# Optimization experiments

Hardware: AMD Instinct MI355X
Metric: run time of the kernel (lower is better)

The kernel has to match this reference:

```python
import jax, jax.numpy as jnp
import numpy as np
from jax import lax

H = 160; W = 160
D_MODEL = 128; D_INNER = 512; D_STATE = 256; NHEADS = 16; HEADDIM = 32
D_CONV = 4; CHUNK = 64
CONV_DIM = D_INNER + 2 * D_STATE            # 1024
D_IN_PROJ = 2 * D_INNER + 2 * D_STATE + NHEADS  # 1552
EPS = 1e-5


def setup_inputs() -> dict:
    key = jax.random.key(0)
    ks = jax.random.split(key, 8)
    nrm = lambda k, s, sc: jax.random.normal(k, s, jnp.float32) * sc
    return {
        "x": jax.random.normal(ks[0], (1, 3, H, W), jnp.float32),
        "fc0_w": nrm(ks[1], (D_MODEL, 3), 0.3),
        "fc0_b": jnp.zeros((D_MODEL,), jnp.float32),
        "in_proj_w": nrm(ks[2], (D_IN_PROJ, D_MODEL), D_MODEL ** -0.5),
        "conv_w": nrm(ks[3], (CONV_DIM, D_CONV), 0.3),
        "conv_b": jnp.zeros((CONV_DIM,), jnp.float32),
        "dt_bias": jnp.log(jnp.expm1(jax.random.uniform(ks[4], (NHEADS,), minval=0.001, maxval=0.1))),
        "A_log": jnp.log(jax.random.uniform(ks[5], (NHEADS,), minval=1.0, maxval=16.0)),
        "D": jnp.ones((NHEADS,), jnp.float32),
        "norm_w": jnp.ones((D_INNER,), jnp.float32),
        "out_proj_w": nrm(ks[6], (D_MODEL, D_INNER), D_INNER ** -0.5),
        "fc1_w": nrm(ks[7], (D_MODEL, H * W), (H * W) ** -0.5),
        "fc1_b": jnp.zeros((D_MODEL,), jnp.float32),
    }


def segsum(x):
    # x: (..., T) -> (..., T, T) with out[i,j] = sum_{j < d <= i} x[d], -inf above diag
    T = x.shape[-1]
    strict = jnp.tril(jnp.ones((T, T), dtype=bool), -1)
    xx = jnp.where(strict, x[..., :, None], 0.0)
    cs = jnp.cumsum(xx, axis=-2)
    keep = jnp.tril(jnp.ones((T, T), dtype=bool))
    return jnp.where(keep, cs, -jnp.inf)


def ssd(xh, A, Bm, Cm):
    # xh: (b,l,h,p) already multiplied by dt; A: (b,l,h) = dt*A_head; Bm,Cm: (b,l,n) (ngroups=1)
    b, l, h, p = xh.shape
    n = Bm.shape[-1]
    c, q = l // CHUNK, CHUNK
    xh = xh.reshape(b, c, q, h, p)
    A = A.reshape(b, c, q, h).transpose(0, 3, 1, 2)          # (b,h,c,q)
    Bm = Bm.reshape(b, c, q, n)
    Cm = Cm.reshape(b, c, q, n)
    A_cs = jnp.cumsum(A, axis=-1)                            # (b,h,c,q)
    Lmat = jnp.exp(segsum(A))                                # (b,h,c,q,q)
    # intra-chunk (quadratic attention-like) term
    Y_diag = jnp.einsum('bcln,bcsn,bhcls,bcshp->bclhp', Cm, Bm, Lmat, xh)
    # per-chunk final states
    decay = jnp.exp(A_cs[..., -1:] - A_cs)                   # (b,h,c,q)
    states = jnp.einsum('bcln,bhcl,bclhp->bchpn', Bm, decay, xh)
    # inter-chunk recurrence: state entering each chunk
    a_tot = jnp.exp(A_cs[..., -1])                           # (b,h,c)
    def step(carry, inp):
        a_c, s_c = inp                                       # (b,h), (b,h,p,n)
        return a_c[..., None, None] * carry + s_c, carry
    _, states_in = lax.scan(step, jnp.zeros((b, h, p, n), xh.dtype),
                            (jnp.moveaxis(a_tot, 2, 0), jnp.moveaxis(states, 1, 0)))
    states_in = jnp.moveaxis(states_in, 0, 1)                # (b,c,h,p,n)
    Y_off = jnp.einsum('bcln,bchpn,bhcl->bclhp', Cm, states_in, jnp.exp(A_cs))
    return (Y_diag + Y_off).reshape(b, l, h, p)


def _forward(x, fc0_w, fc0_b, in_proj_w, conv_w, conv_b, dt_bias, A_log, D,
             norm_w, out_proj_w, fc1_w, fc1_b):
    b = x.shape[0]
    hw = H * W
    # bidirectional pixel flattening
    x1 = x.transpose(0, 2, 3, 1).reshape(b, hw, 3)
    x2 = x[:, :, ::-1, ::-1].transpose(0, 2, 3, 1).reshape(b, hw, 3)
    xc = jnp.concatenate([x1, x2], axis=1)                   # (b, 2*hw, 3)
    u = xc @ fc0_w.T + fc0_b                                 # (b, L, 128)
    L = u.shape[1]
    # Mamba2 in_proj
    zxbcdt = u @ in_proj_w.T                                 # (b, L, 1552)
    z = zxbcdt[..., :D_INNER]
    xBC = zxbcdt[..., D_INNER:D_INNER + CONV_DIM]
    dt = jax.nn.softplus(zxbcdt[..., D_INNER + CONV_DIM:] + dt_bias)  # (b, L, 16)
    # causal depthwise conv1d + silu
    conv = lax.conv_general_dilated(xBC.transpose(0, 2, 1), conv_w[:, None, :],
                                    (1,), [(D_CONV - 1, 0)],
                                    feature_group_count=CONV_DIM,
                                    dimension_numbers=('NCH', 'OIH', 'NCH'))
    xBC = jax.nn.silu(conv + conv_b[None, :, None]).transpose(0, 2, 1)
    xh = xBC[..., :D_INNER].reshape(b, L, NHEADS, HEADDIM)
    Bm = xBC[..., D_INNER:D_INNER + D_STATE]
    Cm = xBC[..., D_INNER + D_STATE:]
    A = -jnp.exp(A_log)                                      # (16,)
    Y = ssd(xh * dt[..., None], dt * A, Bm, Cm)
    Y = Y + D[None, None, :, None] * xh                      # skip connection
    y = Y.reshape(b, L, D_INNER)
    # gated RMSNorm (norm_before_gate=False)
    y = y * jax.nn.silu(z)
    y = y * lax.rsqrt(jnp.mean(y * y, axis=-1, keepdims=True) + EPS) * norm_w
    out = y @ out_proj_w.T                                   # (b, L, 128)
    # second half of sequence, mean over feature dim (AdaptiveAvgPool1d(1))
    half = out[:, hw:, :].mean(axis=-1)                      # (b, hw)
    return half @ fc1_w.T + fc1_b                            # (b, 128)


def reference(x, fc0_w, fc0_b, in_proj_w, conv_w, conv_b, dt_bias, A_log, D,
              norm_w, out_proj_w, fc1_w, fc1_b):
    return _forward(x, fc0_w, fc0_b, in_proj_w, conv_w, conv_b, dt_bias, A_log,
                    D, norm_w, out_proj_w, fc1_w, fc1_b)
```

## Files before the change

kernel.cpp:

```cpp
#include <hip/hip_runtime.h>

#define H_ 160
#define W_ 160
#define HW 25600
#define L_ 51200
#define DM 128
#define DI 512
#define DS 256
#define NH 16
#define HD 32
#define CONVD 1024
#define DIP 1552
#define NCH 800
#define NCH2 400
#define EPSV 1e-5f

typedef __attribute__((ext_vector_type(8))) short bf16x8;
typedef __attribute__((ext_vector_type(8))) unsigned short us8;
typedef __attribute__((ext_vector_type(4))) unsigned short us4;
typedef __attribute__((ext_vector_type(4))) float f32x4;
#define MFMA16(a,b,c) __builtin_amdgcn_mfma_f32_16x16x32_bf16(a,b,c,0,0,0)

__device__ __forceinline__ float b2f(unsigned short u){
  union{unsigned int i; float f;} v; v.i = ((unsigned int)u) << 16; return v.f;
}
__device__ __forceinline__ unsigned short f2b(float f){
  union{unsigned int i; float f;} v; v.f = f;
  unsigned int r = v.i + 0x7fffu + ((v.i >> 16) & 1u);
  return (unsigned short)(r >> 16);
}

__global__ void k_coef(const float* __restrict__ opw, const float* __restrict__ nw,
                       float* __restrict__ coef){
  int i = blockIdx.x * blockDim.x + threadIdx.x;
  if (i >= DI) return;
  float s = 0.f;
  for (int j = 0; j < DM; ++j) s += opw[j * DI + i];
  coef[i] = (s / (float)DM) * nw[i];
}

__global__ __launch_bounds__(256) void k_qtab(const float* __restrict__ ipw,
    const float* __restrict__ fw, const float* __restrict__ fb, float* __restrict__ q){
  int j = blockIdx.x * 256 + threadIdx.x;
  if (j >= DIP) return;
  const float* wr = ipw + (size_t)j * DM;
  float s0 = 0.f, s1 = 0.f, s2 = 0.f, sb = 0.f;
  for (int k = 0; k < DM; ++k){
    float w = wr[k];
    s0 += w * fw[k*3+0]; s1 += w * fw[k*3+1]; s2 += w * fw[k*3+2]; sb += w * fb[k];
  }
  reinterpret_cast<float4*>(q)[j] = make_float4(s0, s1, s2, sb);
}

__device__ __forceinline__ void xrow(const float* __restrict__ x, int l, float* o){
  int i, j;
  if (l < HW){ i = l / W_; j = l % W_; }
  else { int l2 = l - HW; i = (H_ - 1) - l2 / W_; j = (W_ - 1) - l2 % W_; }
  int p = i * W_ + j;
  o[0] = x[p]; o[1] = x[HW + p]; o[2] = x[2*HW + p];
}

__global__ __launch_bounds__(256) void k_fused(const float* __restrict__ x,
    const float* __restrict__ q, const float* __restrict__ cw, const float* __restrict__ cb,
    const float* __restrict__ dt_bias,
    unsigned short* __restrict__ g, unsigned short* __restrict__ xbc, float* __restrict__ dtb){
  int r0 = blockIdx.x * 32;
  int tid = threadIdx.x;
  {
    int c8 = tid & 127, lg = tid >> 7;
    const float4* qv8 = reinterpret_cast<const float4*>(q) + DI + c8 * 8;
    const float4* wv8 = reinterpret_cast<const float4*>(cw) + c8 * 8;
    const float4* cb2 = reinterpret_cast<const float4*>(cb) + c8 * 2;
    float4 bias0 = cb2[0], bias1 = cb2[1];
    float biasv[8] = {bias0.x,bias0.y,bias0.z,bias0.w,bias1.x,bias1.y,bias1.z,bias1.w};
    for (int it = 0; it < 4; ++it){
      int lbase = r0 + (it * 2 + lg) * 4;
      float xv[7][3], vf[7];
      #pragma unroll
      for (int k = 0; k < 7; ++k){
        int l = lbase - 3 + k;
        if (l >= 0){ xrow(x, l, xv[k]); vf[k] = 1.f; }
        else { xv[k][0] = xv[k][1] = xv[k][2] = 0.f; vf[k] = 0.f; }
      }
      unsigned int ow[4][4];
      #pragma unroll
      for (int e = 0; e < 8; ++e){
        float4 qv = qv8[e];
        float raw[7];
        #pragma unroll
        for (int k = 0; k < 7; ++k)
          raw[k] = vf[k]*qv.w + xv[k][0]*qv.x + xv[k][1]*qv.y + xv[k][2]*qv.z;
        float4 wv = wv8[e];
        float bias = biasv[e];
        #pragma unroll
        for (int rr = 0; rr < 4; ++rr){
          float acc = bias + raw[rr]*wv.x + raw[rr+1]*wv.y + raw[rr+2]*wv.z + raw[rr+3]*wv.w;
          float s = acc / (1.f + __expf(-acc));
          unsigned int b = f2b(s);
          if (e & 1) ow[rr][e >> 1] |= b << 16;
          else       ow[rr][e >> 1] = b;
        }
      }
      #pragma unroll
      for (int rr = 0; rr < 4; ++rr){
        uint4 o; o.x = ow[rr][0]; o.y = ow[rr][1]; o.z = ow[rr][2]; o.w = ow[rr][3];
        *reinterpret_cast<uint4*>(xbc + (size_t)(lbase + rr) * CONVD + c8 * 8) = o;
      }
    }
  }
  if (r0 >= HW){
    int c8g = tid & 63;
    const float4* qv8 = reinterpret_cast<const float4*>(q) + c8g * 8;
    for (int it = 0; it < 8; ++it){
      int row = it * 4 + (tid >> 6);
      int l = r0 + row;
      float xv[3]; xrow(x, l, xv);
      unsigned int ow[4];
      #pragma unroll
      for (int e = 0; e < 8; ++e){
        float4 qv = qv8[e];
        float raw = qv.w + xv[0]*qv.x + xv[1]*qv.y + xv[2]*qv.z;
        float s = raw / (1.f + __expf(-raw));
        unsigned int b = f2b(s);
        if (e & 1) ow[e >> 1] |= b << 16;
        else       ow[e >> 1] = b;
      }
      uint4 o; o.x = ow[0]; o.y = ow[1]; o.z = ow[2]; o.w = ow[3];
      *reinterpret_cast<uint4*>(g + (size_t)(l - HW) * DI + c8g * 8) = o;
    }
  }
  {
    int row = tid >> 3, h2 = (tid & 7) * 2;
    int l = r0 + row;
    float xv[3]; xrow(x, l, xv);
    #pragma unroll
    for (int e = 0; e < 2; ++e){
      int h = h2 + e;
      float4 qv = reinterpret_cast<const float4*>(q)[DI + CONVD + h];
      float raw = qv.w + xv[0]*qv.x + xv[1]*qv.y + xv[2]*qv.z + dt_bias[h];
      float sp = (raw > 20.f) ? raw : log1pf(__expf(raw));
      dtb[(size_t)l * NH + h] = sp;
    }
  }
}

__global__ __launch_bounds__(256) void k_chunk(const unsigned short* __restrict__ xbc,
    const float* __restrict__ dtb, const float* __restrict__ A_log,
    unsigned short* __restrict__ states, float* __restrict__ atot,
    float* __restrict__ ecs, unsigned short* __restrict__ ydiag, int cbase){
  __shared__ char U[65536];
  __shared__ float dts[1024];
  __shared__ float Acs[1024];
  unsigned short* Bs = (unsigned short*)U;
  unsigned short* Cs = (unsigned short*)(U + 32768);
  char* Mb  = U;
  char* xdT = U + 8192;
  char* xwT = U + 12288;
  unsigned short* stageS = (unsigned short*)(U + 16384);
  unsigned short* stageY = (unsigned short*)(U + 33280);
  int cl = blockIdx.x, c = cbase + cl, l0 = c * 64;
  int tid = threadIdx.x, lane = tid & 63, wv = tid >> 6;
  int kg = lane >> 4, l15 = lane & 15;
  bool doY = (c >= NCH2);

  for (int i = tid; i < 1024; i += 256) dts[i] = dtb[(size_t)l0 * NH + i];
  #pragma unroll
  for (int it = 0; it < 8; ++it){
    int r = (tid >> 5) + 8 * it, c8 = tid & 31;
    uint4 v = *reinterpret_cast<const uint4*>(xbc + (size_t)(l0 + r) * CONVD + DI + c8 * 8);
    *reinterpret_cast<uint4*>((char*)Bs + ((r * 512 + c8 * 16) ^ ((r & 7) << 4))) = v;
    if (doY){
      uint4 v2 = *reinterpret_cast<const uint4*>(xbc + (size_t)(l0 + r) * CONVD + DI + DS + c8 * 8);
      *reinterpret_cast<uint4*>((char*)Cs + ((r * 512 + c8 * 16) ^ ((r & 7) << 4))) = v2;
    }
  }
  __syncthreads();
  if (tid < 16){
    int h = tid; float Ah = -__expf(A_log[h]); float s = 0.f;
    for (int t = 0; t < 64; ++t){ s += dts[t*16 + h] * Ah; Acs[h*64 + t] = s; }
    atot[c * NH + h] = __expf(s);
  }
  bf16x8 bst[8];
  #pragma unroll
  for (int nt = 0; nt < 4; ++nt)
    #pragma unroll
    for (int s = 0; s < 2; ++s){
      int n = wv * 64 + nt * 16 + l15;
      int tb = s * 32 + kg * 8;
      bf16x8 f;
      #pragma unroll
      for (int e = 0; e < 8; ++e){
        int t = tb + e;
        f[e] = *reinterpret_cast<const short*>((char*)Bs + ((t * 512 + n * 2) ^ ((t & 7) << 4)));
      }
      bst[nt * 2 + s] = f;
    }
  f32x4 Gacc[4];
  if (doY){
    #pragma unroll
    for (int st = 0; st < 4; ++st) Gacc[st] = (f32x4){0.f,0.f,0.f,0.f};
    int trow = wv * 16 + l15;
    for (int ks = 0; ks < 8; ++ks){
      bf16x8 a = *reinterpret_cast<const bf16x8*>((char*)Cs + ((trow * 512 + (ks*32 + kg*8) * 2) ^ ((trow & 7) << 4)));
      #pragma unroll
      for (int st = 0; st < 4; ++st){
        int srow = st * 16 + l15;
        bf16x8 b = *reinterpret_cast<const bf16x8*>((char*)Bs + ((srow * 512 + (ks*32 + kg*8) * 2) ^ ((srow & 7) << 4)));
        Gacc[st] = MFMA16(a, b, Gacc[st]);
      }
    }
  }
  __syncthreads();
  for (int h = 0; h < NH; ++h){
    float alast = Acs[h*64 + 63];
    {
      int t = tid & 63, pb = tid >> 6;
      float dtv = dts[t*16 + h];
      float dec = __expf(alast - Acs[h*64 + t]);
      us8 x8 = *reinterpret_cast<const us8*>(xbc + (size_t)(l0 + t) * CONVD + h * HD + pb * 8);
      #pragma unroll
      for (int e = 0; e < 8; ++e){
        int pp = pb * 8 + e;
        float v = b2f(x8[e]) * dtv;
        if (doY) *reinterpret_cast<unsigned short*>(xdT + ((pp * 128 + t * 2) ^ ((pp & 7) << 4))) = f2b(v);
        *reinterpret_cast<unsigned short*>(xwT + ((pp * 128 + t * 2) ^ ((pp & 7) << 4))) = f2b(v * dec);
      }
    }
    if (doY){
      #pragma unroll
      for (int st = 0; st < 4; ++st)
        #pragma unroll
        for (int r = 0; r < 4; ++r){
          int t = wv * 16 + kg * 4 + r, s2 = st * 16 + l15;
          float m = (s2 <= t) ? Gacc[st][r] * __expf(Acs[h*64 + t] - Acs[h*64 + s2]) : 0.f;
          *reinterpret_cast<unsigned short*>(Mb + ((t * 128 + s2 * 2) ^ ((t & 7) << 4))) = f2b(m);
        }
      if (tid < 64) ecs[((size_t)(c - NCH2) * NH + h) * 64 + tid] = __expf(Acs[h*64 + tid]);
    }
    __syncthreads();
    {
      f32x4 sacc[2][4];
      #pragma unroll
      for (int mt = 0; mt < 2; ++mt)
        #pragma unroll
        for (int nt = 0; nt < 4; ++nt) sacc[mt][nt] = (f32x4){0.f,0.f,0.f,0.f};
      #pragma unroll
      for (int s = 0; s < 2; ++s)
        #pragma unroll
        for (int mt = 0; mt < 2; ++mt){
          int pr = mt * 16 + l15;
          bf16x8 a = *reinterpret_cast<const bf16x8*>(xwT + ((pr * 128 + (s*32 + kg*8) * 2) ^ ((pr & 7) << 4)));
          #pragma unroll
          for (int nt = 0; nt < 4; ++nt) sacc[mt][nt] = MFMA16(a, bst[nt*2 + s], sacc[mt][nt]);
        }
      #pragma unroll
      for (int mt = 0; mt < 2; ++mt)
        #pragma unroll
        for (int nt = 0; nt < 4; ++nt)
          #pragma unroll
          for (int r = 0; r < 4; ++r){
            int pp = mt * 16 + kg * 4 + r, n = wv * 64 + nt * 16 + l15;
            stageS[pp * 264 + n] = f2b(sacc[mt][nt][r]);
          }
    }
    if (doY){
      f32x4 yacc[2];
      yacc[0] = (f32x4){0.f,0.f,0.f,0.f}; yacc[1] = (f32x4){0.f,0.f,0.f,0.f};
      int trow = wv * 16 + l15;
      #pragma unroll
      for (int s = 0; s < 2; ++s){
        bf16x8 a = *reinterpret_cast<const bf16x8*>(Mb + ((trow * 128 + (s*32 + kg*8) * 2) ^ ((trow & 7) << 4)));
        #pragma unroll
        for (int pt = 0; pt < 2; ++pt){
          int pr = pt * 16 + l15;
          bf16x8 b = *reinterpret_cast<const bf16x8*>(xdT + ((pr * 128 + (s*32 + kg*8) * 2) ^ ((pr & 7) << 4)));
          yacc[pt] = MFMA16(a, b, yacc[pt]);
        }
      }
      #pragma unroll
      for (int pt = 0; pt < 2; ++pt)
        #pragma unroll
        for (int r = 0; r < 4; ++r){
          int t = wv * 16 + kg * 4 + r, pp = pt * 16 + l15;
          stageY[t * 40 + pp] = f2b(yacc[pt][r]);
        }
    }
    __syncthreads();
    {
      int row = tid >> 3, seg = tid & 7;
      const unsigned short* sp = stageS + row * 264 + seg * 32;
      unsigned short* gp = states + (((size_t)cl * NH + h) * HD + row) * DS + seg * 32;
      #pragma unroll
      for (int k = 0; k < 4; ++k)
        *reinterpret_cast<uint4*>(gp + k * 8) = *reinterpret_cast<const uint4*>(sp + k * 8);
      if (doY){
        int rw = tid >> 2, quad = tid & 3;
        *reinterpret_cast<uint4*>(ydiag + (size_t)(l0 - HW + rw) * DI + h * HD + quad * 8)
          = *reinterpret_cast<const uint4*>(stageY + rw * 40 + quad * 8);
      }
    }
    __syncthreads();
  }
}

__global__ __launch_bounds__(256) void k_scanred(const unsigned short* __restrict__ states,
    const float* __restrict__ atot, float* __restrict__ carry){
  __shared__ float sat[NCH2];
  int idx = blockIdx.x * 256 + threadIdx.x;
  int h = idx >> 13;
  for (int c = threadIdx.x; c < NCH2; c += 256) sat[c] = atot[c * NH + h];
  __syncthreads();
  float cr = 0.f;
  const unsigned short* p = states + idx;
  for (int c = 0; c < NCH2; ++c){
    cr = sat[c] * cr + b2f(*p);
    p += 131072;
  }
  carry[idx] = cr;
}

__global__ __launch_bounds__(256) void k_scan2(unsigned short* __restrict__ states,
    const float* __restrict__ atot, const float* __restrict__ carry){
  __shared__ float sat[NCH2];
  int idx = blockIdx.x * 256 + threadIdx.x;
  int h = idx >> 13;
  for (int c = threadIdx.x; c < NCH2; c += 256) sat[c] = atot[(NCH2 + c) * NH + h];
  __syncthreads();
  float cr = carry[idx];
  unsigned short* p = states + idx;
  for (int c = 0; c < NCH2; ++c){
    float s = b2f(*p);
    *p = f2b(cr);
    cr = sat[c] * cr + s;
    p += 131072;
  }
}

__global__ __launch_bounds__(256) void k_yoff(const unsigned short* __restrict__ xbc,
    const unsigned short* __restrict__ states, const float* __restrict__ ecs,
    const float* __restrict__ Dv, unsigned short* __restrict__ y,
    const unsigned short* __restrict__ g, float* __restrict__ rms){
  __shared__ unsigned short stage[64 * 520];
  __shared__ float ecs_s[1024];
  int c2 = blockIdx.x;
  int c = c2 + NCH2, l0 = c * 64;
  int tid = threadIdx.x, lane = tid & 63, wv = tid >> 6;
  int kg = lane >> 4, l15 = lane & 15;
  for (int i = tid; i < 1024; i += 256) ecs_s[i] = ecs[(size_t)c2 * 1024 + i];
  bf16x8 aC[8];
  int trow = wv * 16 + l15;
  #pragma unroll
  for (int ks = 0; ks < 8; ++ks)
    aC[ks] = *reinterpret_cast<const bf16x8*>(xbc + (size_t)(l0 + trow) * CONVD + DI + DS + ks * 32 + kg * 8);
  __syncthreads();
  for (int h = 0; h < NH; ++h){
    f32x4 acc[2];
    acc[0] = (f32x4){0.f,0.f,0.f,0.f}; acc[1] = (f32x4){0.f,0.f,0.f,0.f};
    const unsigned short* sb = states + ((size_t)c2 * NH + h) * HD * DS;
    #pragma unroll
    for (int ks = 0; ks < 8; ++ks)
      #pragma unroll
      for (int pt = 0; pt < 2; ++pt){
        bf16x8 b = *reinterpret_cast<const bf16x8*>(sb + (pt * 16 + l15) * DS + ks * 32 + kg * 8);
        acc[pt] = MFMA16(aC[ks], b, acc[pt]);
      }
    float Dh = Dv[h];
    #pragma unroll
    for (int pt = 0; pt < 2; ++pt)
      #pragma unroll
      for (int r = 0; r < 4; ++r){
        int t = wv * 16 + kg * 4 + r, pp = pt * 16 + l15;
        float xh = b2f(xbc[(size_t)(l0 + t) * CONVD + h * HD + pp]);
        stage[t * 520 + h * HD + pp] = f2b(ecs_s[h*64 + t] * acc[pt][r] + Dh * xh);
      }
  }
  __syncthreads();
  int row = tid >> 2, quad = tid & 3;
  const unsigned short* sr = stage + row * 520 + quad * 128;
  size_t obase = (size_t)(c2 * 64 + row) * DI + quad * 128;
  float ss = 0.f;
  #pragma unroll
  for (int k = 0; k < 16; ++k){
    uint4 sv = *reinterpret_cast<const uint4*>(sr + k * 8);
    uint4 yv = *reinterpret_cast<const uint4*>(y + obase + k * 8);
    uint4 gv = *reinterpret_cast<const uint4*>(g + obase + k * 8);
    unsigned int ow[4];
    const unsigned int* svp = (const unsigned int*)&sv;
    const unsigned int* yvp = (const unsigned int*)&yv;
    const unsigned int* gvp = (const unsigned int*)&gv;
    #pragma unroll
    for (int e = 0; e < 4; ++e){
      float v0 = b2f((unsigned short)(svp[e] & 0xffff)) + b2f((unsigned short)(yvp[e] & 0xffff));
      float v1 = b2f((unsigned short)(svp[e] >> 16)) + b2f((unsigned short)(yvp[e] >> 16));
      float y0 = v0 * b2f((unsigned short)(gvp[e] & 0xffff));
      float y1 = v1 * b2f((unsigned short)(gvp[e] >> 16));
      ss += y0 * y0 + y1 * y1;
      ow[e] = (unsigned int)f2b(y0) | ((unsigned int)f2b(y1) << 16);
    }
    uint4 o; o.x = ow[0]; o.y = ow[1]; o.z = ow[2]; o.w = ow[3];
    *reinterpret_cast<uint4*>(y + obase + k * 8) = o;
  }
  ss += __shfl_xor(ss, 1, 64);
  ss += __shfl_xor(ss, 2, 64);
  if (quad == 0) rms[c2 * 64 + row] = rsqrtf(ss / (float)DI + EPSV);
}

__global__ __launch_bounds__(256) void k_half(const unsigned short* __restrict__ yg,
    const float* __restrict__ rms, const float* __restrict__ coef,
    float* __restrict__ half_out){
  int wave = threadIdx.x >> 6, lane = threadIdx.x & 63;
  int row = blockIdx.x * 4 + wave;
  if (row >= HW) return;
  const unsigned short* yr = yg + (size_t)row * DI;
  float acc = 0.f;
  for (int i = lane; i < DI; i += 64) acc += b2f(yr[i]) * coef[i];
  #pragma unroll
  for (int off = 32; off; off >>= 1) acc += __shfl_down(acc, off, 64);
  if (lane == 0) half_out[row] = acc * rms[row];
}

__global__ __launch_bounds__(256) void k_fc1(const float* __restrict__ half_in,
    const float* __restrict__ w, const float* __restrict__ b, float* __restrict__ out){
  int k = blockIdx.x;
  const float* wr = w + (size_t)k * HW;
  float acc = 0.f;
  for (int i = threadIdx.x; i < HW; i += 256) acc += half_in[i] * wr[i];
  __shared__ float red[256];
  red[threadIdx.x] = acc;
  __syncthreads();
  for (int s = 128; s; s >>= 1){
    if (threadIdx.x < s) red[threadIdx.x] += red[threadIdx.x + s];
    __syncthreads();
  }
  if (threadIdx.x == 0) out[k] = red[0] + b[k];
}

extern "C" void kernel_launch(void* const* d_in, const int* in_sizes, int n_in,
                              void* d_out, int out_size, void* d_ws, size_t ws_size,
                              hipStream_t stream){
  const float* x      = (const float*)d_in[0];
  const float* fc0_w  = (const float*)d_in[1];
  const float* fc0_b  = (const float*)d_in[2];
  const float* ipw    = (const float*)d_in[3];
  const float* conv_w = (const float*)d_in[4];
  const float* conv_b = (const float*)d_in[5];
  const float* dt_bias= (const float*)d_in[6];
  const float* A_log  = (const float*)d_in[7];
  const float* Dv     = (const float*)d_in[8];
  const float* norm_w = (const float*)d_in[9];
  const float* opw    = (const float*)d_in[10];
  const float* fc1_w  = (const float*)d_in[11];
  const float* fc1_b  = (const float*)d_in[12];
  float* out = (float*)d_out;

  char* ws = (char*)d_ws;
  size_t off = 0;
  float* dtb          = (float*)(ws + off);           off += (size_t)L_ * NH * 4;
  unsigned short* stx = (unsigned short*)(ws + off);  off += (size_t)L_ * CONVD * 2;
  unsigned short* xbc = (unsigned short*)(ws + off);  off += (size_t)L_ * CONVD * 2;
  unsigned short* g   = (unsigned short*)(ws + off);  off += (size_t)HW * DI * 2;
  unsigned short* yd  = (unsigned short*)(ws + off);  off += (size_t)HW * DI * 2;
  float* atot         = (float*)(ws + off);           off += (size_t)NCH * NH * 4;
  float* ecs          = (float*)(ws + off);           off += (size_t)NCH2 * NH * 64 * 4;
  float* rms          = (float*)(ws + off);           off += (size_t)HW * 4;
  float* half_buf     = (float*)(ws + off);           off += (size_t)HW * 4;
  float* coef         = (float*)(ws + off);           off += (size_t)DI * 4;
  float* carry        = (float*)(ws + off);           off += (size_t)131072 * 4;
  float* qtab         = (float*)(ws + off);           off += (size_t)DIP * 4 * 4;

  if (ws_size < off) return;

  k_coef   <<<2, 256, 0, stream>>>(opw, norm_w, coef);
  k_qtab   <<<(DIP + 255) / 256, 256, 0, stream>>>(ipw, fc0_w, fc0_b, qtab);
  k_fused  <<<L_ / 32, 256, 0, stream>>>(x, qtab, conv_w, conv_b, dt_bias, g, xbc, dtb);
  k_chunk  <<<NCH2, 256, 0, stream>>>(xbc, dtb, A_log, stx, atot, ecs, yd, 0);
  k_scanred<<<512, 256, 0, stream>>>(stx, atot, carry);
  k_chunk  <<<NCH2, 256, 0, stream>>>(xbc, dtb, A_log, stx, atot, ecs, yd, NCH2);
  k_scan2  <<<512, 256, 0, stream>>>(stx, atot, carry);
  k_yoff   <<<NCH2, 256, 0, stream>>>(xbc, stx, ecs, Dv, yd, g, rms);
  k_half   <<<HW / 4, 256, 0, stream>>>(yd, rms, coef, half_buf);
  k_fc1    <<<DM, 256, 0, stream>>>(half_buf, fc1_w, fc1_b, out);
}
```

Before: 489.2 us.

## Recompute gate in yoff instead of storing it, vectorize scan kernels

The z-gate tensor g is no longer written by k_fused and read back in k_yoff. k_yoff now recomputes silu(z) from x and the projection table held in shared memory, which removes a 26 MB bf16 round trip at the cost of extra exp work per element. k_fused is relaunched with 16 rows per block, so it has twice as many blocks. The two scan kernels now process four state elements per thread with vector loads and stores, using a quarter of the blocks. That gives wider memory accesses but fewer concurrent threads on what is a latency-bound sequential loop.

```diff
diff --git a/kernel.cpp b/kernel.cpp
--- a/kernel.cpp
+++ b/kernel.cpp
@@ -63,8 +63,8 @@
 __global__ __launch_bounds__(256) void k_fused(const float* __restrict__ x,
     const float* __restrict__ q, const float* __restrict__ cw, const float* __restrict__ cb,
     const float* __restrict__ dt_bias,
-    unsigned short* __restrict__ g, unsigned short* __restrict__ xbc, float* __restrict__ dtb){
-  int r0 = blockIdx.x * 32;
+    unsigned short* __restrict__ xbc, float* __restrict__ dtb){
+  int r0 = blockIdx.x * 16;
   int tid = threadIdx.x;
   {
     int c8 = tid & 127, lg = tid >> 7;
@@ -73,7 +73,7 @@
     const float4* cb2 = reinterpret_cast<const float4*>(cb) + c8 * 2;
     float4 bias0 = cb2[0], bias1 = cb2[1];
     float biasv[8] = {bias0.x,bias0.y,bias0.z,bias0.w,bias1.x,bias1.y,bias1.z,bias1.w};
-    for (int it = 0; it < 4; ++it){
+    for (int it = 0; it < 2; ++it){
       int lbase = r0 + (it * 2 + lg) * 4;
       float xv[7][3], vf[7];
       #pragma unroll
@@ -108,39 +108,14 @@
       }
     }
   }
-  if (r0 >= HW){
-    int c8g = tid & 63;
-    const float4* qv8 = reinterpret_cast<const float4*>(q) + c8g * 8;
-    for (int it = 0; it < 8; ++it){
-      int row = it * 4 + (tid >> 6);
-      int l = r0 + row;
-      float xv[3]; xrow(x, l, xv);
-      unsigned int ow[4];
-      #pragma unroll
-      for (int e = 0; e < 8; ++e){
-        float4 qv = qv8[e];
-        float raw = qv.w + xv[0]*qv.x + xv[1]*qv.y + xv[2]*qv.z;
-        float s = raw / (1.f + __expf(-raw));
-        unsigned int b = f2b(s);
-        if (e & 1) ow[e >> 1] |= b << 16;
-        else       ow[e >> 1] = b;
-      }
-      uint4 o; o.x = ow[0]; o.y = ow[1]; o.z = ow[2]; o.w = ow[3];
-      *reinterpret_cast<uint4*>(g + (size_t)(l - HW) * DI + c8g * 8) = o;
-    }
-  }
   {
-    int row = tid >> 3, h2 = (tid & 7) * 2;
+    int row = tid >> 4, h = tid & 15;
     int l = r0 + row;
     float xv[3]; xrow(x, l, xv);
-    #pragma unroll
-    for (int e = 0; e < 2; ++e){
-      int h = h2 + e;
-      float4 qv = reinterpret_cast<const float4*>(q)[DI + CONVD + h];
-      float raw = qv.w + xv[0]*qv.x + xv[1]*qv.y + xv[2]*qv.z + dt_bias[h];
-      float sp = (raw > 20.f) ? raw : log1pf(__expf(raw));
-      dtb[(size_t)l * NH + h] = sp;
-    }
+    float4 qv = reinterpret_cast<const float4*>(q)[DI + CONVD + h];
+    float raw = qv.w + xv[0]*qv.x + xv[1]*qv.y + xv[2]*qv.z + dt_bias[h];
+    float sp = (raw > 20.f) ? raw : log1pf(__expf(raw));
+    dtb[(size_t)l * NH + h] = sp;
   }
 }
 
@@ -307,31 +282,45 @@
     const float* __restrict__ atot, float* __restrict__ carry){
   __shared__ float sat[NCH2];
   int idx = blockIdx.x * 256 + threadIdx.x;
-  int h = idx >> 13;
+  int base = idx * 4;
+  int h = base >> 13;
   for (int c = threadIdx.x; c < NCH2; c += 256) sat[c] = atot[c * NH + h];
   __syncthreads();
-  float cr = 0.f;
-  const unsigned short* p = states + idx;
+  float cr0 = 0.f, cr1 = 0.f, cr2 = 0.f, cr3 = 0.f;
+  const unsigned short* p = states + base;
   for (int c = 0; c < NCH2; ++c){
-    cr = sat[c] * cr + b2f(*p);
+    us4 v = *reinterpret_cast<const us4*>(p);
+    float a = sat[c];
+    cr0 = a * cr0 + b2f(v[0]);
+    cr1 = a * cr1 + b2f(v[1]);
+    cr2 = a * cr2 + b2f(v[2]);
+    cr3 = a * cr3 + b2f(v[3]);
     p += 131072;
   }
-  carry[idx] = cr;
+  f32x4 o = {cr0, cr1, cr2, cr3};
+  *reinterpret_cast<f32x4*>(carry + base) = o;
 }
 
 __global__ __launch_bounds__(256) void k_scan2(unsigned short* __restrict__ states,
     const float* __restrict__ atot, const float* __restrict__ carry){
   __shared__ float sat[NCH2];
   int idx = blockIdx.x * 256 + threadIdx.x;
-  int h = idx >> 13;
+  int base = idx * 4;
+  int h = base >> 13;
   for (int c = threadIdx.x; c < NCH2; c += 256) sat[c] = atot[(NCH2 + c) * NH + h];
   __syncthreads();
-  float cr = carry[idx];
-  unsigned short* p = states + idx;
+  f32x4 crv = *reinterpret_cast<const f32x4*>(carry + base);
+  float cr0 = crv[0], cr1 = crv[1], cr2 = crv[2], cr3 = crv[3];
+  unsigned short* p = states + base;
   for (int c = 0; c < NCH2; ++c){
-    float s = b2f(*p);
-    *p = f2b(cr);
-    cr = sat[c] * cr + s;
+    us4 v = *reinterpret_cast<const us4*>(p);
+    us4 o; o[0] = f2b(cr0); o[1] = f2b(cr1); o[2] = f2b(cr2); o[3] = f2b(cr3);
+    *reinterpret_cast<us4*>(p) = o;
+    float a = sat[c];
+    cr0 = a * cr0 + b2f(v[0]);
+    cr1 = a * cr1 + b2f(v[1]);
+    cr2 = a * cr2 + b2f(v[2]);
+    cr3 = a * cr3 + b2f(v[3]);
     p += 131072;
   }
 }
@@ -339,14 +328,17 @@
 __global__ __launch_bounds__(256) void k_yoff(const unsigned short* __restrict__ xbc,
     const unsigned short* __restrict__ states, const float* __restrict__ ecs,
     const float* __restrict__ Dv, unsigned short* __restrict__ y,
-    const unsigned short* __restrict__ g, float* __restrict__ rms){
+    const float* __restrict__ x, const float* __restrict__ qtab,
+    float* __restrict__ rms){
   __shared__ unsigned short stage[64 * 520];
   __shared__ float ecs_s[1024];
+  __shared__ float4 qs[DI];
   int c2 = blockIdx.x;
   int c = c2 + NCH2, l0 = c * 64;
   int tid = threadIdx.x, lane = tid & 63, wv = tid >> 6;
   int kg = lane >> 4, l15 = lane & 15;
   for (int i = tid; i < 1024; i += 256) ecs_s[i] = ecs[(size_t)c2 * 1024 + i];
+  for (int i = tid; i < DI; i += 256) qs[i] = reinterpret_cast<const float4*>(qtab)[i];
   bf16x8 aC[8];
   int trow = wv * 16 + l15;
   #pragma unroll
@@ -376,6 +368,7 @@
   }
   __syncthreads();
   int row = tid >> 2, quad = tid & 3;
+  float xv[3]; xrow(x, l0 + row, xv);
   const unsigned short* sr = stage + row * 520 + quad * 128;
   size_t obase = (size_t)(c2 * 64 + row) * DI + quad * 128;
   float ss = 0.f;
@@ -383,17 +376,21 @@
   for (int k = 0; k < 16; ++k){
     uint4 sv = *reinterpret_cast<const uint4*>(sr + k * 8);
     uint4 yv = *reinterpret_cast<const uint4*>(y + obase + k * 8);
-    uint4 gv = *reinterpret_cast<const uint4*>(g + obase + k * 8);
     unsigned int ow[4];
     const unsigned int* svp = (const unsigned int*)&sv;
     const unsigned int* yvp = (const unsigned int*)&yv;
-    const unsigned int* gvp = (const unsigned int*)&gv;
     #pragma unroll
     for (int e = 0; e < 4; ++e){
+      int j0 = quad * 128 + k * 8 + e * 2;
+      float4 q0 = qs[j0], q1 = qs[j0 + 1];
+      float z0 = q0.w + xv[0]*q0.x + xv[1]*q0.y + xv[2]*q0.z;
+      float z1 = q1.w + xv[0]*q1.x + xv[1]*q1.y + xv[2]*q1.z;
+      float g0 = z0 / (1.f + __expf(-z0));
+      float g1 = z1 / (1.f + __expf(-z1));
       float v0 = b2f((unsigned short)(svp[e] & 0xffff)) + b2f((unsigned short)(yvp[e] & 0xffff));
       float v1 = b2f((unsigned short)(svp[e] >> 16)) + b2f((unsigned short)(yvp[e] >> 16));
-      float y0 = v0 * b2f((unsigned short)(gvp[e] & 0xffff));
-      float y1 = v1 * b2f((unsigned short)(gvp[e] >> 16));
+      float y0 = v0 * g0;
+      float y1 = v1 * g1;
       ss += y0 * y0 + y1 * y1;
       ow[e] = (unsigned int)f2b(y0) | ((unsigned int)f2b(y1) << 16);
     }
@@ -458,7 +455,6 @@
   float* dtb          = (float*)(ws + off);           off += (size_t)L_ * NH * 4;
   unsigned short* stx = (unsigned short*)(ws + off);  off += (size_t)L_ * CONVD * 2;
   unsigned short* xbc = (unsigned short*)(ws + off);  off += (size_t)L_ * CONVD * 2;
-  unsigned short* g   = (unsigned short*)(ws + off);  off += (size_t)HW * DI * 2;
   unsigned short* yd  = (unsigned short*)(ws + off);  off += (size_t)HW * DI * 2;
   float* atot         = (float*)(ws + off);           off += (size_t)NCH * NH * 4;
   float* ecs          = (float*)(ws + off);           off += (size_t)NCH2 * NH * 64 * 4;
@@ -472,12 +468,12 @@
 
   k_coef   <<<2, 256, 0, stream>>>(opw, norm_w, coef);
   k_qtab   <<<(DIP + 255) / 256, 256, 0, stream>>>(ipw, fc0_w, fc0_b, qtab);
-  k_fused  <<<L_ / 32, 256, 0, stream>>>(x, qtab, conv_w, conv_b, dt_bias, g, xbc, dtb);
+  k_fused  <<<L_ / 16, 256, 0, stream>>>(x, qtab, conv_w, conv_b, dt_bias, xbc, dtb);
   k_chunk  <<<NCH2, 256, 0, stream>>>(xbc, dtb, A_log, stx, atot, ecs, yd, 0);
-  k_scanred<<<512, 256, 0, stream>>>(stx, atot, carry);
+  k_scanred<<<128, 256, 0, stream>>>(stx, atot, carry);
   k_chunk  <<<NCH2, 256, 0, stream>>>(xbc, dtb, A_log, stx, atot, ecs, yd, NCH2);
-  k_scan2  <<<512, 256, 0, stream>>>(stx, atot, carry);
-  k_yoff   <<<NCH2, 256, 0, stream>>>(xbc, stx, ecs, Dv, yd, g, rms);
+  k_scan2  <<<128, 256, 0, stream>>>(stx, atot, carry);
+  k_yoff   <<<NCH2, 256, 0, stream>>>(xbc, stx, ecs, Dv, yd, x, qtab, rms);
   k_half   <<<HW / 4, 256, 0, stream>>>(yd, rms, coef, half_buf);
   k_fc1    <<<DM, 256, 0, stream>>>(half_buf, fc1_w, fc1_b, out);
 }
```

Result: slower. 550.8 us (+12.6%).
